# Performance work log

Hardware: AMD Instinct MI355X
Metric: run time of the kernel (lower is better)

Reference implementation:

```python
import jax, jax.numpy as jnp
import numpy as np
import math

B, S, D, H = 1, 4096, 1024, 16
DH = D // H  # head_dim = 64
NEG = -10000.0  # matches torch masked-fill value in source (not -inf)


def setup_inputs() -> dict:
    key = jax.random.key(0)
    ks = jax.random.split(key, 5)
    scale = 0.02
    return {
        "x": jax.random.normal(ks[0], (B, S, D), dtype=jnp.float32),
        "Wqkv_w": jax.random.normal(ks[1], (3 * D, D), dtype=jnp.float32) * scale,
        "Wqkv_b": jax.random.normal(ks[2], (3 * D,), dtype=jnp.float32) * scale,
        "out_w": jax.random.normal(ks[3], (D, D), dtype=jnp.float32) * scale,
        "out_b": jax.random.normal(ks[4], (D,), dtype=jnp.float32) * scale,
    }


def reference(x, Wqkv_w, Wqkv_b, out_w, out_b):
    # QKV projection: (B,S,D) @ (D,3D) + b -> (B,S,3,H,DH)
    qkv = jnp.einsum('bsd,ed->bse', x, Wqkv_w) + Wqkv_b
    qkv = qkv.reshape(B, S, 3, H, DH)
    q, k, v = qkv[:, :, 0], qkv[:, :, 1], qkv[:, :, 2]  # each (B,S,H,DH)
    softmax_scale = 1.0 / math.sqrt(DH)
    # scores: (B,H,T,S)
    scores = jnp.einsum('bthd,bshd->bhts', q, k * softmax_scale)
    # causal additive mask with -10000 above diagonal (faithful to source)
    causal_mask = jnp.triu(jnp.full((S, S), NEG, dtype=scores.dtype), k=1)
    scores = scores + causal_mask
    attention = jax.nn.softmax(scores, axis=-1)
    context = jnp.einsum('bhts,bshd->bthd', attention, v)  # (B,T,H,DH)
    context = context.reshape(B, S, D)
    out = jnp.einsum('bsd,ed->bse', context, out_w) + out_b
    return out
```

## Files before the change

### kernel.cpp

```cpp
#include <hip/hip_runtime.h>
#include <hip/hip_bf16.h>

using f32x4  = __attribute__((ext_vector_type(4))) float;
using f32x16 = __attribute__((ext_vector_type(16))) float;
using bf16x8 = __attribute__((ext_vector_type(8))) __bf16;
using u16x8  = __attribute__((ext_vector_type(8))) unsigned short;
using u32x4  = __attribute__((ext_vector_type(4))) unsigned int;

#define DEV __device__ __forceinline__

constexpr int S_  = 4096;
constexpr int D_  = 1024;
constexpr int KD  = 1024;

constexpr size_t XB_OFF   = 0;
constexpr size_t WQKV_OFF = 8388608;
constexpr size_t WOUT_OFF = 14680064;
constexpr size_t QB_OFF   = 16777216;
constexpr size_t KB_OFF   = 25165824;
constexpr size_t VT_OFF   = 33554432;
constexpr size_t CTX_OFF  = 41943040;

DEV unsigned short f2bf(float f) {
  __hip_bfloat16 h = __float2bfloat16(f);
  return __builtin_bit_cast(unsigned short, h);
}

DEV void gl_lds16(const void* g, void* l) {
  __builtin_amdgcn_global_load_lds(
      (const __attribute__((address_space(1))) void*)g,
      (__attribute__((address_space(3))) void*)l, 16, 0, 0);
}

DEV f32x4 mfma16(bf16x8 a, bf16x8 b, f32x4 c) {
  return __builtin_amdgcn_mfma_f32_16x16x32_bf16(a, b, c, 0, 0, 0);
}
DEV f32x16 mfma32(bf16x8 a, bf16x8 b, f32x16 c) {
  return __builtin_amdgcn_mfma_f32_32x32x16_bf16(a, b, c, 0, 0, 0);
}
DEV unsigned cvtpk(float lo, float hi) {
  unsigned r;
  asm("v_cvt_pk_bf16_f32 %0, %1, %2" : "=v"(r) : "v"(lo), "v"(hi));
  return r;
}
DEV float exp2_fast(float x) {
  float r;
  asm("v_exp_f32 %0, %1" : "=v"(r) : "v"(x));
  return r;
}
DEV void pl32(unsigned& a, unsigned& b) {
  asm("v_permlane32_swap_b32 %0, %1" : "+v"(a), "+v"(b));
}
DEV float xhalf_max(float x) {
  float y;
  asm("v_mov_b32 %0, %1" : "=v"(y) : "v"(x));
  unsigned a = __builtin_bit_cast(unsigned, x), b = __builtin_bit_cast(unsigned, y);
  pl32(a, b);
  return fmaxf(__builtin_bit_cast(float, a), __builtin_bit_cast(float, b));
}
DEV float xhalf_add(float x) {
  float y;
  asm("v_mov_b32 %0, %1" : "=v"(y) : "v"(x));
  unsigned a = __builtin_bit_cast(unsigned, x), b = __builtin_bit_cast(unsigned, y);
  pl32(a, b);
  return __builtin_bit_cast(float, a) + __builtin_bit_cast(float, b);
}

__global__ void cvt_k(const float* __restrict__ s, unsigned short* __restrict__ d, int n8) {
  int i = blockIdx.x * 256 + threadIdx.x;
  if (i >= n8) return;
  const float4* s4 = (const float4*)s;
  float4 a = s4[2 * i], b = s4[2 * i + 1];
  u16x8 o;
  o[0] = f2bf(a.x); o[1] = f2bf(a.y); o[2] = f2bf(a.z); o[3] = f2bf(a.w);
  o[4] = f2bf(b.x); o[5] = f2bf(b.y); o[6] = f2bf(b.z); o[7] = f2bf(b.w);
  ((u16x8*)d)[i] = o;
}

template <int EPI>
__global__ __launch_bounds__(256)
void gemm_bt_k(const unsigned short* __restrict__ A,
               const unsigned short* __restrict__ Bt,
               const float* __restrict__ bias,
               unsigned short* __restrict__ qb,
               unsigned short* __restrict__ kb,
               unsigned short* __restrict__ vt,
               float* __restrict__ outf) {
  __shared__ unsigned short As[128 * 32];
  __shared__ unsigned short Bs[128 * 32];
  const int t = threadIdx.x;
  const int w = t >> 6, l = t & 63;
  const int lr = l & 15, lg = l >> 4, lk = lg * 8;
  const int m0 = blockIdx.y * 128, n0 = blockIdx.x * 128;
  const int wm = (w >> 1) * 64, wn = (w & 1) * 64;

  f32x4 acc[4][4] = {};

  const int srow = t >> 2;
  const int scolb = (t & 3) << 4;
  const char* Ag = (const char*)A + (size_t)(m0 + srow) * (KD * 2) + scolb;
  const char* Bg = (const char*)Bt + (size_t)(n0 + srow) * (KD * 2) + scolb;
  char* AsB = (char*)As;
  char* BsB = (char*)Bs;

  for (int kt = 0; kt < KD / 32; ++kt) {
    const char* ak = Ag + kt * 64;
    const char* bk = Bg + kt * 64;
    gl_lds16(ak,                 AsB + t * 16);
    gl_lds16(ak + 64 * (KD * 2), AsB + 4096 + t * 16);
    gl_lds16(bk,                 BsB + t * 16);
    gl_lds16(bk + 64 * (KD * 2), BsB + 4096 + t * 16);
    __syncthreads();

    bf16x8 a[4], b[4];
#pragma unroll
    for (int mi = 0; mi < 4; ++mi)
      a[mi] = *(const bf16x8*)&As[(wm + mi * 16 + lr) * 32 + lk];
#pragma unroll
    for (int ni = 0; ni < 4; ++ni)
      b[ni] = *(const bf16x8*)&Bs[(wn + ni * 16 + lr) * 32 + lk];
#pragma unroll
    for (int mi = 0; mi < 4; ++mi)
#pragma unroll
      for (int ni = 0; ni < 4; ++ni)
        acc[mi][ni] = mfma16(a[mi], b[ni], acc[mi][ni]);
    __syncthreads();
  }

  const int r0 = lg * 4;
  if (EPI == 0) {
    const int which = n0 >> 10;
    const float kscale = 0.125f * 1.44269504088896f;
#pragma unroll
    for (int mi = 0; mi < 4; ++mi) {
      const int sbase = m0 + wm + mi * 16 + r0;
#pragma unroll
      for (int ni = 0; ni < 4; ++ni) {
        const int e = n0 + wn + ni * 16 + lr;
        const float bv = bias[e];
        const int h = (e & 1023) >> 6, dd = e & 63;
#pragma unroll
        for (int r = 0; r < 4; ++r) {
          const float v = acc[mi][ni][r] + bv;
          const int sr = sbase + r;
          if (which == 0)      qb[((size_t)(h * S_ + sr)) * 64 + dd] = f2bf(v);
          else if (which == 1) kb[((size_t)(h * S_ + sr)) * 64 + dd] = f2bf(v * kscale);
          else                 vt[((size_t)(h * 64 + dd)) * S_ + sr] = f2bf(v);
        }
      }
    }
  } else {
#pragma unroll
    for (int mi = 0; mi < 4; ++mi) {
      const int sbase = m0 + wm + mi * 16 + r0;
#pragma unroll
      for (int ni = 0; ni < 4; ++ni) {
        const int e = n0 + wn + ni * 16 + lr;
        const float bv = bias[e];
#pragma unroll
        for (int r = 0; r < 4; ++r)
          outf[(size_t)(sbase + r) * D_ + e] = acc[mi][ni][r] + bv;
      }
    }
  }
}

__global__ __launch_bounds__(512, 2)
void attn_k(const unsigned short* __restrict__ Qb,
            const unsigned short* __restrict__ Kb,
            const unsigned short* __restrict__ Vt,
            unsigned short* __restrict__ ctx) {
  __shared__ char smem[65536];

  const int t = threadIdx.x;
  const int w8 = t >> 6;
  const int g  = w8 >> 2;
  const int w  = w8 & 3;
  const int l = t & 63, lq = l & 31, hi = l >> 5;
  const int pairIdx = blockIdx.x;
  const int h = blockIdx.y;

  const int sg = t >> 8;
  const int ts = t & 255;
  const int srow = ts >> 3;
  const int ssw  = ((ts & 7) << 4) ^ ((srow & 7) << 4);
  const char* Kg0 = (const char*)Kb + (size_t)(h * S_) * 128;
  const char* Vg0 = (const char*)Vt + (size_t)(h * 64) * (size_t)(S_ * 2);

  for (int task = 0; task < 2; ++task) {
    const int bi = task == 0 ? (31 - pairIdx) : pairIdx;
    const int q0 = bi * 128;
    const int qrow = q0 + w * 32 + lq;
    const int qwmin = q0 + w * 32, qwmax = qwmin + 31;
    const int niter = bi + 1;

    const unsigned short* Qr = Qb + ((size_t)(h * S_ + qrow)) * 64;
    bf16x8 qf[4];
#pragma unroll
    for (int d0 = 0; d0 < 4; ++d0)
      qf[d0] = *(const bf16x8*)(Qr + d0 * 16 + hi * 8);

    f32x16 cacc[2] = {};
    float m = -INFINITY, lsum = 0.f;

    auto stage = [&](int buf, int it) {
      const int kv0 = (it + sg * niter) * 64;
      char* kd = smem + sg * 16384 + buf * 8192;
      const char* Kg = Kg0 + (size_t)kv0 * 128;
      gl_lds16(Kg + (size_t)srow * 128 + ssw,        kd + ts * 16);
      gl_lds16(Kg + (size_t)(32 + srow) * 128 + ssw, kd + 4096 + ts * 16);
      char* vd = smem + 32768 + sg * 16384 + buf * 8192;
      const char* Vg = Vg0 + (size_t)kv0 * 2;
      gl_lds16(Vg + (size_t)srow * (S_ * 2) + ssw,        vd + ts * 16);
      gl_lds16(Vg + (size_t)(32 + srow) * (S_ * 2) + ssw, vd + 4096 + ts * 16);
    };

    int cur = 0;
    stage(0, 0);

    for (int it = 0; it < niter; ++it) {
      __syncthreads();
      if (it + 1 < niter) stage(cur ^ 1, it + 1);
      const char* Kt = smem + g * 16384 + cur * 8192;
      const char* Vl = smem + 32768 + g * 16384 + cur * 8192;
      const int tt = it + g * niter;

#pragma unroll
      for (int kvh = 0; kvh < 2; ++kvh) {
        const int kv0s = tt * 64 + kvh * 32;
        if (kv0s > qwmax) continue;

        f32x16 st = {};
        const int kr = kvh * 32 + lq;
        const char* kbase = Kt + kr * 128;
        const int ksw = (kr & 7) << 4;
#pragma unroll
        for (int d0 = 0; d0 < 4; ++d0) {
          bf16x8 kf = *(const bf16x8*)(kbase + ((d0 * 32 + hi * 16) ^ ksw));
          st = mfma32(kf, qf[d0], st);
        }

        if (kv0s + 31 > qwmin) {
#pragma unroll
          for (int r = 0; r < 16; ++r) {
            const int kvg = kv0s + (r & 3) + 8 * (r >> 2) + 4 * hi;
            if (kvg > qrow) st[r] = -INFINITY;
          }
        }

        float pmax = st[0];
#pragma unroll
        for (int r = 1; r < 16; ++r) pmax = fmaxf(pmax, st[r]);
        pmax = xhalf_max(pmax);

        if (!__all(pmax <= m)) {
          const float mnew = fmaxf(m, pmax);
          const float alpha = exp2_fast(m - mnew);
          lsum *= alpha;
#pragma unroll
          for (int j = 0; j < 16; ++j) { cacc[0][j] *= alpha; cacc[1][j] *= alpha; }
          m = mnew;
        }

        float p[16];
        float rs = 0.f;
#pragma unroll
        for (int r = 0; r < 16; ++r) { p[r] = exp2_fast(st[r] - m); rs += p[r]; }
        lsum += xhalf_add(rs);

        unsigned x0 = cvtpk(p[0], p[1]),  x1 = cvtpk(p[2], p[3]);
        unsigned y0 = cvtpk(p[4], p[5]),  y1 = cvtpk(p[6], p[7]);
        pl32(x0, y0); pl32(x1, y1);
        u32x4 f0 = {x0, x1, y0, y1};
        bf16x8 pf0 = __builtin_bit_cast(bf16x8, f0);
        unsigned x2 = cvtpk(p[8], p[9]),   x3 = cvtpk(p[10], p[11]);
        unsigned y2 = cvtpk(p[12], p[13]), y3 = cvtpk(p[14], p[15]);
        pl32(x2, y2); pl32(x3, y3);
        u32x4 f1 = {x2, x3, y2, y3};
        bf16x8 pf1 = __builtin_bit_cast(bf16x8, f1);

#pragma unroll
        for (int db = 0; db < 2; ++db) {
          const int dr = db * 32 + lq;
          const char* vbase = Vl + dr * 128;
          const int vsw = (dr & 7) << 4;
          bf16x8 v0 = *(const bf16x8*)(vbase + ((kvh * 64 + hi * 16) ^ vsw));
          bf16x8 v1 = *(const bf16x8*)(vbase + ((kvh * 64 + 32 + hi * 16) ^ vsw));
          cacc[db] = mfma32(v0, pf0, cacc[db]);
          cacc[db] = mfma32(v1, pf1, cacc[db]);
        }
      }
      cur ^= 1;
    }

    __syncthreads();
    float* comb = (float*)smem;
    float* slot = comb + (size_t)(w * 64 + l) * 36;
    if (g == 1) {
      slot[0] = m; slot[1] = lsum;
#pragma unroll
      for (int j = 0; j < 16; ++j) { slot[4 + j] = cacc[0][j]; slot[20 + j] = cacc[1][j]; }
    }
    __syncthreads();
    if (g == 0) {
      const float m1 = slot[0], l1 = slot[1];
      const float M = fmaxf(m, m1);
      const float a0 = exp2_fast(m - M), a1 = exp2_fast(m1 - M);
      const float inv = 1.0f / (lsum * a0 + l1 * a1);
      const float s0 = a0 * inv, s1 = a1 * inv;
      unsigned short* base = ctx + (size_t)qrow * D_ + h * 64;
#pragma unroll
      for (int db = 0; db < 2; ++db)
#pragma unroll
        for (int r = 0; r < 16; r += 2) {
          const float o0 = cacc[db][r]     * s0 + slot[4 + db * 16 + r]     * s1;
          const float o1 = cacc[db][r + 1] * s0 + slot[4 + db * 16 + r + 1] * s1;
          const unsigned wv = cvtpk(o0, o1);
          const int d = (r & 3) + 8 * (r >> 2) + 4 * hi + 32 * db;
          *(unsigned*)(base + d) = wv;
        }
    }
    __syncthreads();
  }
}

extern "C" void kernel_launch(void* const* d_in, const int* in_sizes, int n_in,
                              void* d_out, int out_size, void* d_ws, size_t ws_size,
                              hipStream_t stream) {
  const float* x      = (const float*)d_in[0];
  const float* Wqkv_w = (const float*)d_in[1];
  const float* Wqkv_b = (const float*)d_in[2];
  const float* out_w  = (const float*)d_in[3];
  const float* out_b  = (const float*)d_in[4];
  float* out = (float*)d_out;
  char* ws = (char*)d_ws;

  unsigned short* xb    = (unsigned short*)(ws + XB_OFF);
  unsigned short* wqkvb = (unsigned short*)(ws + WQKV_OFF);
  unsigned short* woutb = (unsigned short*)(ws + WOUT_OFF);
  unsigned short* Qb    = (unsigned short*)(ws + QB_OFF);
  unsigned short* Kb    = (unsigned short*)(ws + KB_OFF);
  unsigned short* Vt    = (unsigned short*)(ws + VT_OFF);
  unsigned short* ctx   = (unsigned short*)(ws + CTX_OFF);

  cvt_k<<<2048, 256, 0, stream>>>(x, xb, 4096 * 1024 / 8);
  cvt_k<<<1536, 256, 0, stream>>>(Wqkv_w, wqkvb, 3072 * 1024 / 8);
  cvt_k<<<512, 256, 0, stream>>>(out_w, woutb, 1024 * 1024 / 8);

  gemm_bt_k<0><<<dim3(24, 32), 256, 0, stream>>>(xb, wqkvb, Wqkv_b, Qb, Kb, Vt, nullptr);

  attn_k<<<dim3(16, 16), 512, 0, stream>>>(Qb, Kb, Vt, ctx);

  gemm_bt_k<1><<<dim3(8, 32), 256, 0, stream>>>(ctx, woutb, out_b, nullptr, nullptr, nullptr, out);
}
```

Before: 139.2 us.

## Split attention KV across four wave groups, read V from global, double-buffer GEMM

The attention kernel now uses 1024-thread blocks with four wave groups that interleave KV tiles, so each group processes every fourth tile. Their partial softmax states are merged through shared memory in a tree reduction. V is read directly from global memory instead of being staged in LDS, which frees LDS for K double-buffering per group but adds uncoalesced global loads. The GEMM gets double-buffered LDS with one barrier per k-step, overlapping the next tile's load with the current compute.

After: 175.0 us. +25.8%, slower.

```diff
diff --git a/kernel.cpp b/kernel.cpp
--- a/kernel.cpp
+++ b/kernel.cpp
@@ -86,8 +86,8 @@
                unsigned short* __restrict__ kb,
                unsigned short* __restrict__ vt,
                float* __restrict__ outf) {
-  __shared__ unsigned short As[128 * 32];
-  __shared__ unsigned short Bs[128 * 32];
+  __shared__ unsigned short As[2][4096];
+  __shared__ unsigned short Bs[2][4096];
   const int t = threadIdx.x;
   const int w = t >> 6, l = t & 63;
   const int lr = l & 15, lg = l >> 4, lk = lg * 8;
@@ -100,31 +100,36 @@
   const int scolb = (t & 3) << 4;
   const char* Ag = (const char*)A + (size_t)(m0 + srow) * (KD * 2) + scolb;
   const char* Bg = (const char*)Bt + (size_t)(n0 + srow) * (KD * 2) + scolb;
-  char* AsB = (char*)As;
-  char* BsB = (char*)Bs;
-
-  for (int kt = 0; kt < KD / 32; ++kt) {
+
+  auto stage = [&](int buf, int kt) {
     const char* ak = Ag + kt * 64;
     const char* bk = Bg + kt * 64;
+    char* AsB = (char*)&As[buf][0];
+    char* BsB = (char*)&Bs[buf][0];
     gl_lds16(ak,                 AsB + t * 16);
     gl_lds16(ak + 64 * (KD * 2), AsB + 4096 + t * 16);
     gl_lds16(bk,                 BsB + t * 16);
     gl_lds16(bk + 64 * (KD * 2), BsB + 4096 + t * 16);
-    __syncthreads();
+  };
+
+  stage(0, 0);
+  for (int kt = 0; kt < KD / 32; ++kt) {
+    __syncthreads();
+    if (kt + 1 < KD / 32) stage((kt + 1) & 1, kt + 1);
+    const int buf = kt & 1;
 
     bf16x8 a[4], b[4];
 #pragma unroll
     for (int mi = 0; mi < 4; ++mi)
-      a[mi] = *(const bf16x8*)&As[(wm + mi * 16 + lr) * 32 + lk];
+      a[mi] = *(const bf16x8*)&As[buf][(wm + mi * 16 + lr) * 32 + lk];
 #pragma unroll
     for (int ni = 0; ni < 4; ++ni)
-      b[ni] = *(const bf16x8*)&Bs[(wn + ni * 16 + lr) * 32 + lk];
+      b[ni] = *(const bf16x8*)&Bs[buf][(wn + ni * 16 + lr) * 32 + lk];
 #pragma unroll
     for (int mi = 0; mi < 4; ++mi)
 #pragma unroll
       for (int ni = 0; ni < 4; ++ni)
         acc[mi][ni] = mfma16(a[mi], b[ni], acc[mi][ni]);
-    __syncthreads();
   }
 
   const int r0 = lg * 4;
@@ -165,7 +170,7 @@
   }
 }
 
-__global__ __launch_bounds__(512, 2)
+__global__ __launch_bounds__(1024, 4)
 void attn_k(const unsigned short* __restrict__ Qb,
             const unsigned short* __restrict__ Kb,
             const unsigned short* __restrict__ Vt,
@@ -173,26 +178,26 @@
   __shared__ char smem[65536];
 
   const int t = threadIdx.x;
-  const int w8 = t >> 6;
-  const int g  = w8 >> 2;
-  const int w  = w8 & 3;
+  const int w16 = t >> 6;
+  const int w = w16 & 3;
+  const int g = w16 >> 2;
   const int l = t & 63, lq = l & 31, hi = l >> 5;
   const int pairIdx = blockIdx.x;
   const int h = blockIdx.y;
 
-  const int sg = t >> 8;
   const int ts = t & 255;
   const int srow = ts >> 3;
   const int ssw  = ((ts & 7) << 4) ^ ((srow & 7) << 4);
   const char* Kg0 = (const char*)Kb + (size_t)(h * S_) * 128;
-  const char* Vg0 = (const char*)Vt + (size_t)(h * 64) * (size_t)(S_ * 2);
+  const unsigned short* Vh = Vt + (size_t)(h * 64) * S_;
 
   for (int task = 0; task < 2; ++task) {
     const int bi = task == 0 ? (31 - pairIdx) : pairIdx;
     const int q0 = bi * 128;
     const int qrow = q0 + w * 32 + lq;
     const int qwmin = q0 + w * 32, qwmax = qwmin + 31;
-    const int niter = bi + 1;
+    const int ntiles = 2 * bi + 2;
+    const int maxit = (ntiles + 3) >> 2;
 
     const unsigned short* Qr = Qb + ((size_t)(h * S_ + qrow)) * 64;
     bf16x8 qf[4];
@@ -203,119 +208,129 @@
     f32x16 cacc[2] = {};
     float m = -INFINITY, lsum = 0.f;
 
-    auto stage = [&](int buf, int it) {
-      const int kv0 = (it + sg * niter) * 64;
-      char* kd = smem + sg * 16384 + buf * 8192;
-      const char* Kg = Kg0 + (size_t)kv0 * 128;
+    auto stageK = [&](int buf, int tl) {
+      char* kd = smem + g * 16384 + buf * 8192;
+      const char* Kg = Kg0 + (size_t)(tl * 64) * 128;
       gl_lds16(Kg + (size_t)srow * 128 + ssw,        kd + ts * 16);
       gl_lds16(Kg + (size_t)(32 + srow) * 128 + ssw, kd + 4096 + ts * 16);
-      char* vd = smem + 32768 + sg * 16384 + buf * 8192;
-      const char* Vg = Vg0 + (size_t)kv0 * 2;
-      gl_lds16(Vg + (size_t)srow * (S_ * 2) + ssw,        vd + ts * 16);
-      gl_lds16(Vg + (size_t)(32 + srow) * (S_ * 2) + ssw, vd + 4096 + ts * 16);
     };
 
-    int cur = 0;
-    stage(0, 0);
-
-    for (int it = 0; it < niter; ++it) {
+    if (g < ntiles) stageK(0, g);
+
+    for (int it = 0; it < maxit; ++it) {
       __syncthreads();
-      if (it + 1 < niter) stage(cur ^ 1, it + 1);
-      const char* Kt = smem + g * 16384 + cur * 8192;
-      const char* Vl = smem + 32768 + g * 16384 + cur * 8192;
-      const int tt = it + g * niter;
-
-#pragma unroll
-      for (int kvh = 0; kvh < 2; ++kvh) {
-        const int kv0s = tt * 64 + kvh * 32;
-        if (kv0s > qwmax) continue;
-
-        f32x16 st = {};
-        const int kr = kvh * 32 + lq;
-        const char* kbase = Kt + kr * 128;
-        const int ksw = (kr & 7) << 4;
-#pragma unroll
-        for (int d0 = 0; d0 < 4; ++d0) {
-          bf16x8 kf = *(const bf16x8*)(kbase + ((d0 * 32 + hi * 16) ^ ksw));
-          st = mfma32(kf, qf[d0], st);
-        }
-
-        if (kv0s + 31 > qwmin) {
-#pragma unroll
-          for (int r = 0; r < 16; ++r) {
-            const int kvg = kv0s + (r & 3) + 8 * (r >> 2) + 4 * hi;
-            if (kvg > qrow) st[r] = -INFINITY;
+      const int tl = it * 4 + g;
+      if (tl + 4 < ntiles) stageK((it + 1) & 1, tl + 4);
+      if (tl < ntiles) {
+        const int kv0 = tl * 64;
+        const char* Kt = smem + g * 16384 + (it & 1) * 8192;
+
+#pragma unroll
+        for (int kvh = 0; kvh < 2; ++kvh) {
+          const int kv0s = kv0 + kvh * 32;
+          if (kv0s > qwmax) continue;
+
+          f32x16 st = {};
+          const int kr = kvh * 32 + lq;
+          const char* kbase = Kt + kr * 128;
+          const int ksw = (kr & 7) << 4;
+#pragma unroll
+          for (int d0 = 0; d0 < 4; ++d0) {
+            bf16x8 kf = *(const bf16x8*)(kbase + ((d0 * 32 + hi * 16) ^ ksw));
+            st = mfma32(kf, qf[d0], st);
+          }
+
+          if (kv0s + 31 > qwmin) {
+#pragma unroll
+            for (int r = 0; r < 16; ++r) {
+              const int kvg = kv0s + (r & 3) + 8 * (r >> 2) + 4 * hi;
+              if (kvg > qrow) st[r] = -INFINITY;
+            }
+          }
+
+          float pmax = st[0];
+#pragma unroll
+          for (int r = 1; r < 16; ++r) pmax = fmaxf(pmax, st[r]);
+          pmax = xhalf_max(pmax);
+
+          if (!__all(pmax <= m)) {
+            const float mnew = fmaxf(m, pmax);
+            const float alpha = exp2_fast(m - mnew);
+            lsum *= alpha;
+#pragma unroll
+            for (int j = 0; j < 16; ++j) { cacc[0][j] *= alpha; cacc[1][j] *= alpha; }
+            m = mnew;
+          }
+
+          float rs = 0.f;
+#pragma unroll
+          for (int r = 0; r < 16; ++r) { st[r] = exp2_fast(st[r] - m); rs += st[r]; }
+          lsum += xhalf_add(rs);
+
+          unsigned x0 = cvtpk(st[0], st[1]),   x1 = cvtpk(st[2], st[3]);
+          unsigned y0 = cvtpk(st[4], st[5]),   y1 = cvtpk(st[6], st[7]);
+          pl32(x0, y0); pl32(x1, y1);
+          u32x4 f0 = {x0, x1, y0, y1};
+          bf16x8 pf0 = __builtin_bit_cast(bf16x8, f0);
+          unsigned x2 = cvtpk(st[8], st[9]),   x3 = cvtpk(st[10], st[11]);
+          unsigned y2 = cvtpk(st[12], st[13]), y3 = cvtpk(st[14], st[15]);
+          pl32(x2, y2); pl32(x3, y3);
+          u32x4 f1 = {x2, x3, y2, y3};
+          bf16x8 pf1 = __builtin_bit_cast(bf16x8, f1);
+
+#pragma unroll
+          for (int db = 0; db < 2; ++db) {
+            const unsigned short* vr =
+                Vh + (size_t)(db * 32 + lq) * S_ + kv0s + hi * 8;
+            bf16x8 v0 = *(const bf16x8*)(vr);
+            bf16x8 v1 = *(const bf16x8*)(vr + 16);
+            cacc[db] = mfma32(v0, pf0, cacc[db]);
+            cacc[db] = mfma32(v1, pf1, cacc[db]);
           }
         }
-
-        float pmax = st[0];
-#pragma unroll
-        for (int r = 1; r < 16; ++r) pmax = fmaxf(pmax, st[r]);
-        pmax = xhalf_max(pmax);
-
-        if (!__all(pmax <= m)) {
-          const float mnew = fmaxf(m, pmax);
-          const float alpha = exp2_fast(m - mnew);
-          lsum *= alpha;
-#pragma unroll
-          for (int j = 0; j < 16; ++j) { cacc[0][j] *= alpha; cacc[1][j] *= alpha; }
-          m = mnew;
-        }
-
-        float p[16];
-        float rs = 0.f;
-#pragma unroll
-        for (int r = 0; r < 16; ++r) { p[r] = exp2_fast(st[r] - m); rs += p[r]; }
-        lsum += xhalf_add(rs);
-
-        unsigned x0 = cvtpk(p[0], p[1]),  x1 = cvtpk(p[2], p[3]);
-        unsigned y0 = cvtpk(p[4], p[5]),  y1 = cvtpk(p[6], p[7]);
-        pl32(x0, y0); pl32(x1, y1);
-        u32x4 f0 = {x0, x1, y0, y1};
-        bf16x8 pf0 = __builtin_bit_cast(bf16x8, f0);
-        unsigned x2 = cvtpk(p[8], p[9]),   x3 = cvtpk(p[10], p[11]);
-        unsigned y2 = cvtpk(p[12], p[13]), y3 = cvtpk(p[14], p[15]);
-        pl32(x2, y2); pl32(x3, y3);
-        u32x4 f1 = {x2, x3, y2, y3};
-        bf16x8 pf1 = __builtin_bit_cast(bf16x8, f1);
-
-#pragma unroll
-        for (int db = 0; db < 2; ++db) {
-          const int dr = db * 32 + lq;
-          const char* vbase = Vl + dr * 128;
-          const int vsw = (dr & 7) << 4;
-          bf16x8 v0 = *(const bf16x8*)(vbase + ((kvh * 64 + hi * 16) ^ vsw));
-          bf16x8 v1 = *(const bf16x8*)(vbase + ((kvh * 64 + 32 + hi * 16) ^ vsw));
-          cacc[db] = mfma32(v0, pf0, cacc[db]);
-          cacc[db] = mfma32(v1, pf1, cacc[db]);
-        }
       }
-      cur ^= 1;
     }
 
-    __syncthreads();
-    float* comb = (float*)smem;
-    float* slot = comb + (size_t)(w * 64 + l) * 36;
-    if (g == 1) {
+    float* slot = (float*)smem + (size_t)(w * 64 + l) * 37;
+    auto writeP = [&]() {
       slot[0] = m; slot[1] = lsum;
 #pragma unroll
-      for (int j = 0; j < 16; ++j) { slot[4 + j] = cacc[0][j]; slot[20 + j] = cacc[1][j]; }
-    }
+      for (int j = 0; j < 16; ++j) { slot[2 + j] = cacc[0][j]; slot[18 + j] = cacc[1][j]; }
+    };
+    auto mergeP = [&]() {
+      const float m2 = slot[0], l2 = slot[1];
+      const float M = fmaxf(m, m2);
+      const float a1 = (m  == -INFINITY) ? 0.f : exp2_fast(m - M);
+      const float a2 = (m2 == -INFINITY) ? 0.f : exp2_fast(m2 - M);
+      lsum = lsum * a1 + l2 * a2;
+#pragma unroll
+      for (int j = 0; j < 16; ++j) {
+        cacc[0][j] = cacc[0][j] * a1 + slot[2 + j]  * a2;
+        cacc[1][j] = cacc[1][j] * a1 + slot[18 + j] * a2;
+      }
+      m = M;
+    };
+
+    __syncthreads();
+    if (g == 1) writeP();
+    __syncthreads();
+    if (g == 0) mergeP();
+    __syncthreads();
+    if (g == 3) writeP();
+    __syncthreads();
+    if (g == 2) mergeP();
+    __syncthreads();
+    if (g == 2) writeP();
     __syncthreads();
     if (g == 0) {
-      const float m1 = slot[0], l1 = slot[1];
-      const float M = fmaxf(m, m1);
-      const float a0 = exp2_fast(m - M), a1 = exp2_fast(m1 - M);
-      const float inv = 1.0f / (lsum * a0 + l1 * a1);
-      const float s0 = a0 * inv, s1 = a1 * inv;
+      mergeP();
+      const float inv = 1.0f / lsum;
       unsigned short* base = ctx + (size_t)qrow * D_ + h * 64;
 #pragma unroll
       for (int db = 0; db < 2; ++db)
 #pragma unroll
         for (int r = 0; r < 16; r += 2) {
-          const float o0 = cacc[db][r]     * s0 + slot[4 + db * 16 + r]     * s1;
-          const float o1 = cacc[db][r + 1] * s0 + slot[4 + db * 16 + r + 1] * s1;
-          const unsigned wv = cvtpk(o0, o1);
+          const unsigned wv = cvtpk(cacc[db][r] * inv, cacc[db][r + 1] * inv);
           const int d = (r & 3) + 8 * (r >> 2) + 4 * hi + 32 * db;
           *(unsigned*)(base + d) = wv;
         }
@@ -349,7 +364,7 @@
 
   gemm_bt_k<0><<<dim3(24, 32), 256, 0, stream>>>(xb, wqkvb, Wqkv_b, Qb, Kb, Vt, nullptr);
 
-  attn_k<<<dim3(16, 16), 512, 0, stream>>>(Qb, Kb, Vt, ctx);
+  attn_k<<<dim3(16, 16), 1024, 0, stream>>>(Qb, Kb, Vt, ctx);
 
   gemm_bt_k<1><<<dim3(8, 32), 256, 0, stream>>>(ctx, woutb, out_b, nullptr, nullptr, nullptr, out);
 }
```
